# Kernel tuning notes

Hardware: AMD Instinct MI355X
Metric: run time of the kernel (lower is better)

Reference implementation:

```python
import jax, jax.numpy as jnp
import numpy as np

K = 7      # kernel_size
PAD = 3    # padding ('same' with stride 1)
G = 16     # groups


def _unfold(x):
    """torch nn.Unfold equivalent, stride=1, dilation=1.
    Returns [B, C, K*K, H, W] with kernel positions ordered (kh, kw),
    matching torch's (c, kh, kw) channel-major layout after reshape."""
    B, C, H, W = x.shape
    xp = jnp.pad(x, ((0, 0), (0, 0), (PAD, PAD), (PAD, PAD)))
    patches = jnp.stack(
        [xp[:, :, i:i + H, j:j + W] for i in range(K) for j in range(K)],
        axis=2,
    )
    return patches


def setup_inputs() -> dict:
    key = jax.random.key(0)
    k1, k2, k3 = jax.random.split(key, 3)
    B, C, H, W = 4, 256, 64, 64
    x = jax.random.normal(k1, (B, C, H, W), dtype=jnp.float32)
    # 1x1 conv producing kernel_prod*groups = 49*16 = 784 channels (with bias)
    w_kernel = jax.random.normal(k2, (G * K * K, C), dtype=jnp.float32) * 0.05
    b_kernel = jax.random.normal(k3, (G * K * K,), dtype=jnp.float32) * 0.05
    return {"x": x, "w_kernel": w_kernel, "b_kernel": b_kernel}


def reference(x, w_kernel, b_kernel):
    B, C, H, W = x.shape
    Cg = C // G
    # unfolded input: [B, G, C//G, K*K, H, W]
    patches = _unfold(x).reshape(B, G, Cg, K * K, H, W)
    # dynamic per-pixel kernel: AvgPool(k=1) is identity at stride 1,
    # then 1x1 conv with bias -> [B, G*K*K, H, W]
    kern = jnp.einsum('bchw,kc->bkhw', x, w_kernel) + b_kernel[None, :, None, None]
    kern = kern.reshape(B, G, 1, K * K, H, W)
    # multiply and sum-reduce over kernel positions, flatten groups
    out = (patches * kern).sum(axis=3).reshape(B, C, H, W)
    return out
```

## Files before the change

kernel.cpp:

```cpp
#include <hip/hip_runtime.h>


#define B_   4
#define C_   256
#define G_   16
#define KK_  49
#define KS_  7
#define PD_  3

#define XT_BYTES  (B_*4096*C_*2)
#define WBF_OFF   XT_BYTES

#define SKW   28
#define HC_   70
#define HPOS  (10*HC_)

typedef __attribute__((ext_vector_type(8))) short bf16x8;
typedef __attribute__((ext_vector_type(4))) float f32x4;
typedef unsigned short ushort_t;

__device__ inline unsigned f2bf(float f) {
    unsigned u = __float_as_uint(f);
    u += 0x7FFF + ((u >> 16) & 1);
    return u >> 16;
}

__global__ __launch_bounds__(256)
void cvt_xT(const float* __restrict__ x, const float* __restrict__ wk,
            ushort_t* __restrict__ xT, unsigned* __restrict__ wbf) {
    const int t = threadIdx.x;
    if (blockIdx.x == 64) {
        const int slice = blockIdx.z * 4 + blockIdx.y;
        const float2* wk2 = (const float2*)wk;
        const int base = slice * 6272;
        for (int k = t; k < 6272; k += 256) {
            float2 v = wk2[base + k];
            wbf[base + k] = f2bf(v.x) | (f2bf(v.y) << 16);
        }
        return;
    }
    __shared__ float tile[64][65];
    const int p0 = blockIdx.x * 64;
    const int c0 = blockIdx.y * 64;
    const int b  = blockIdx.z;
    const int px_r = t & 63;
    #pragma unroll
    for (int i = 0; i < 16; ++i) {
        int ch = (t >> 6) + i * 4;
        tile[ch][px_r] = x[((size_t)(b * C_ + c0 + ch) << 12) + p0 + px_r];
    }
    __syncthreads();
    const int px  = t >> 2;
    const int seg = t & 3;
    unsigned u[8];
    #pragma unroll
    for (int j = 0; j < 8; ++j) {
        float a0 = tile[seg * 16 + 2 * j][px];
        float a1 = tile[seg * 16 + 2 * j + 1][px];
        u[j] = f2bf(a0) | (f2bf(a1) << 16);
    }
    unsigned* dst = (unsigned*)(xT + ((size_t)((b << 12) + p0 + px)) * C_ + c0 + seg * 16);
    ((uint4*)dst)[0] = make_uint4(u[0], u[1], u[2], u[3]);
    ((uint4*)dst)[1] = make_uint4(u[4], u[5], u[6], u[7]);
}

__global__ __launch_bounds__(256, 4)
void inv_fused(const ushort_t* __restrict__ xT,
               const ushort_t* __restrict__ wbf,
               const float* __restrict__ bk,
               const float* __restrict__ x,
               float* __restrict__ out) {
    __shared__ unsigned kern2[256 * SKW];
    __shared__ unsigned halo4[HPOS * 4];

    const int bid  = blockIdx.x;
    const int g    = bid >> 6;
    const int b    = (bid >> 4) & 3;
    const int tile = bid & 15;
    const int gy0  = tile * 4;
    const int p0   = gy0 * 64;

    const int tid  = threadIdx.x;
    const int wv   = tid >> 6;
    const int ln15 = tid & 15;
    const int quad = (tid & 63) >> 4;

    f32x4 acc[16];
    #pragma unroll
    for (int i = 0; i < 16; ++i) acc[i] = (f32x4){0.f, 0.f, 0.f, 0.f};

    const ushort_t* ap[4];
    #pragma unroll
    for (int mt = 0; mt < 4; ++mt) {
        int r = mt * 16 + ln15; if (r > KK_ - 1) r = KK_ - 1;
        ap[mt] = wbf + (size_t)(g * KK_ + r) * C_ + quad * 8;
    }
    const ushort_t* bp = xT + ((size_t)((b << 12) + p0 + wv * 64 + ln15)) * C_ + quad * 8;

    bf16x8 af[2][4], bf[2][4];
    #pragma unroll
    for (int mt = 0; mt < 4; ++mt) af[0][mt] = *(const bf16x8*)(ap[mt]);
    #pragma unroll
    for (int nt = 0; nt < 4; ++nt) bf[0][nt] = *(const bf16x8*)(bp + nt * 16 * C_);

    #pragma unroll
    for (int k = 0; k < 8; ++k) {
        const int cur = k & 1, nxt = cur ^ 1;
        if (k < 7) {
            const int cc = (k + 1) * 32;
            #pragma unroll
            for (int mt = 0; mt < 4; ++mt)
                af[nxt][mt] = *(const bf16x8*)(ap[mt] + cc);
            #pragma unroll
            for (int nt = 0; nt < 4; ++nt)
                bf[nxt][nt] = *(const bf16x8*)(bp + nt * 16 * C_ + cc);
        }
        #pragma unroll
        for (int mt = 0; mt < 4; ++mt) {
            #pragma unroll
            for (int nt = 0; nt < 4; ++nt) {
                acc[mt * 4 + nt] = __builtin_amdgcn_mfma_f32_16x16x32_bf16(
                    af[cur][mt], bf[cur][nt], acc[mt * 4 + nt], 0, 0, 0);
            }
        }
    }

    #pragma unroll
    for (int mt = 0; mt < 3; ++mt) {
        const int m0 = mt * 16 + quad * 4;
        const float b0 = bk[g * KK_ + m0],     b1 = bk[g * KK_ + m0 + 1];
        const float b2 = bk[g * KK_ + m0 + 2], b3 = bk[g * KK_ + m0 + 3];
        #pragma unroll
        for (int nt = 0; nt < 4; ++nt) {
            const int p = wv * 64 + nt * 16 + ln15;
            uint2 d;
            d.x = f2bf(acc[mt * 4 + nt][0] + b0) | (f2bf(acc[mt * 4 + nt][1] + b1) << 16);
            d.y = f2bf(acc[mt * 4 + nt][2] + b2) | (f2bf(acc[mt * 4 + nt][3] + b3) << 16);
            *(uint2*)&kern2[p * SKW + mt * 8 + quad * 2] = d;
        }
    }
    if (quad == 0) {
        const float b48 = bk[g * KK_ + 48];
        #pragma unroll
        for (int nt = 0; nt < 4; ++nt) {
            const int p = wv * 64 + nt * 16 + ln15;
            kern2[p * SKW + 24] = f2bf(acc[12 + nt][0] + b48);
        }
    }
    __syncthreads();

    float kv[KK_];
    {
        const uint4* kr = (const uint4*)&kern2[tid * SKW];
        unsigned kd[28];
        #pragma unroll
        for (int q = 0; q < 7; ++q) {
            uint4 h = kr[q];
            kd[4*q] = h.x; kd[4*q+1] = h.y; kd[4*q+2] = h.z; kd[4*q+3] = h.w;
        }
        #pragma unroll
        for (int k = 0; k < KK_; ++k) {
            unsigned d = kd[k >> 1];
            kv[k] = __uint_as_float((k & 1) ? (d & 0xffff0000u) : (d << 16));
        }
    }

    const int py = tid >> 6, px = tid & 63;
    #pragma unroll 1
    for (int hb = 0; hb < 2; ++hb) {
        if (hb) __syncthreads();
        const int cbase = g * 16 + hb * 8;
        for (int e = tid; e < HPOS; e += 256) {
            int row = e / HC_;
            int col = e - row * HC_;
            int sy = gy0 + row - PD_;
            int sx = col - PD_;
            unsigned d0 = 0, d1 = 0, d2 = 0, d3 = 0;
            if (sy >= 0 && sy < 64 && sx >= 0 && sx < 64) {
                const float* xp = x + ((size_t)(b * C_ + cbase) << 12) + sy * 64 + sx;
                d0 = f2bf(xp[0])             | (f2bf(xp[1 << 12]) << 16);
                d1 = f2bf(xp[2 << 12])       | (f2bf(xp[3 << 12]) << 16);
                d2 = f2bf(xp[4 << 12])       | (f2bf(xp[5 << 12]) << 16);
                d3 = f2bf(xp[6 << 12])       | (f2bf(xp[7 << 12]) << 16);
            }
            *(uint4*)&halo4[e * 4] = make_uint4(d0, d1, d2, d3);
        }
        __syncthreads();

        float a[8];
        #pragma unroll
        for (int q = 0; q < 8; ++q) a[q] = 0.f;
        #pragma unroll
        for (int kh = 0; kh < KS_; ++kh) {
            const uint4* hr = (const uint4*)&halo4[(((py + kh) * HC_) + px) * 4];
            #pragma unroll
            for (int kw = 0; kw < KS_; ++kw) {
                uint4 hv = hr[kw];
                float kk = kv[kh * KS_ + kw];
                a[0] = fmaf(__uint_as_float(hv.x << 16),          kk, a[0]);
                a[1] = fmaf(__uint_as_float(hv.x & 0xffff0000u),  kk, a[1]);
                a[2] = fmaf(__uint_as_float(hv.y << 16),          kk, a[2]);
                a[3] = fmaf(__uint_as_float(hv.y & 0xffff0000u),  kk, a[3]);
                a[4] = fmaf(__uint_as_float(hv.z << 16),          kk, a[4]);
                a[5] = fmaf(__uint_as_float(hv.z & 0xffff0000u),  kk, a[5]);
                a[6] = fmaf(__uint_as_float(hv.w << 16),          kk, a[6]);
                a[7] = fmaf(__uint_as_float(hv.w & 0xffff0000u),  kk, a[7]);
            }
        }
        const size_t o = ((size_t)(b * C_ + cbase) << 12) + p0 + tid;
        #pragma unroll
        for (int q = 0; q < 8; ++q)
            out[o + ((size_t)q << 12)] = a[q];
    }
}

extern "C" void kernel_launch(void* const* d_in, const int* in_sizes, int n_in,
                              void* d_out, int out_size, void* d_ws, size_t ws_size,
                              hipStream_t stream) {
    const float* x  = (const float*)d_in[0];
    const float* wk = (const float*)d_in[1];
    const float* bk = (const float*)d_in[2];
    float* o = (float*)d_out;

    ushort_t* xT  = (ushort_t*)d_ws;
    unsigned* wbf = (unsigned*)((char*)d_ws + WBF_OFF);

    cvt_xT<<<dim3(65, 4, B_), dim3(256), 0, stream>>>(x, wk, xT, wbf);
    inv_fused<<<dim3(1024), dim3(256), 0, stream>>>(
        xT, (const ushort_t*)wbf, bk, x, o);
}
```

Before: 117.7 us.

## Halve pixel tile, load all 16 group channels in one halo pass

Each block now covers 2 output rows (128 pixels) instead of 4, so the grid doubles to 2048 blocks. The two threads per pixel split the 16 group channels into halves, and a single halo tile holds all 16 channels, which removes the second halo load and its extra barriers. The halo load now runs before the kernel-weight epilogue to overlap global loads with MFMA results, and launch bounds rise to 5 blocks per CU. In exchange, halo rows overlap more across tiles (8 rows per 2 output rows instead of 10 per 4), adding redundant x reads, and the weight matrix is re-read per smaller tile.

Result: slower. 128.4 us (+9.2%).

```diff
diff --git a/kernel.cpp b/kernel.cpp
--- a/kernel.cpp
+++ b/kernel.cpp
@@ -13,7 +13,8 @@
 
 #define SKW   28
 #define HC_   70
-#define HPOS  (10*HC_)
+#define HROWS 8
+#define HPOS  (HROWS*HC_)
 
 typedef __attribute__((ext_vector_type(8))) short bf16x8;
 typedef __attribute__((ext_vector_type(4))) float f32x4;
@@ -64,30 +65,31 @@
     ((uint4*)dst)[1] = make_uint4(u[4], u[5], u[6], u[7]);
 }
 
-__global__ __launch_bounds__(256, 4)
+__global__ __launch_bounds__(256, 5)
 void inv_fused(const ushort_t* __restrict__ xT,
                const ushort_t* __restrict__ wbf,
                const float* __restrict__ bk,
                const float* __restrict__ x,
                float* __restrict__ out) {
-    __shared__ unsigned kern2[256 * SKW];
-    __shared__ unsigned halo4[HPOS * 4];
+    __shared__ unsigned kern2[128 * SKW];
+    __shared__ unsigned halo8[HPOS * 8];
 
     const int bid  = blockIdx.x;
-    const int g    = bid >> 6;
-    const int b    = (bid >> 4) & 3;
-    const int tile = bid & 15;
-    const int gy0  = tile * 4;
-    const int p0   = gy0 * 64;
+    const int g    = bid >> 7;
+    const int rem  = bid & 127;
+    const int b    = rem >> 5;
+    const int tile = rem & 31;
+    const int gy0  = tile * 2;
+    const int p0   = tile * 128;
 
     const int tid  = threadIdx.x;
     const int wv   = tid >> 6;
     const int ln15 = tid & 15;
     const int quad = (tid & 63) >> 4;
 
-    f32x4 acc[16];
-    #pragma unroll
-    for (int i = 0; i < 16; ++i) acc[i] = (f32x4){0.f, 0.f, 0.f, 0.f};
+    f32x4 acc[8];
+    #pragma unroll
+    for (int i = 0; i < 8; ++i) acc[i] = (f32x4){0.f, 0.f, 0.f, 0.f};
 
     const ushort_t* ap[4];
     #pragma unroll
@@ -95,13 +97,13 @@
         int r = mt * 16 + ln15; if (r > KK_ - 1) r = KK_ - 1;
         ap[mt] = wbf + (size_t)(g * KK_ + r) * C_ + quad * 8;
     }
-    const ushort_t* bp = xT + ((size_t)((b << 12) + p0 + wv * 64 + ln15)) * C_ + quad * 8;
-
-    bf16x8 af[2][4], bf[2][4];
+    const ushort_t* bp = xT + ((size_t)((b << 12) + p0 + wv * 32 + ln15)) * C_ + quad * 8;
+
+    bf16x8 af[2][4], bf[2][2];
     #pragma unroll
     for (int mt = 0; mt < 4; ++mt) af[0][mt] = *(const bf16x8*)(ap[mt]);
     #pragma unroll
-    for (int nt = 0; nt < 4; ++nt) bf[0][nt] = *(const bf16x8*)(bp + nt * 16 * C_);
+    for (int nt = 0; nt < 2; ++nt) bf[0][nt] = *(const bf16x8*)(bp + nt * 16 * C_);
 
     #pragma unroll
     for (int k = 0; k < 8; ++k) {
@@ -112,17 +114,35 @@
             for (int mt = 0; mt < 4; ++mt)
                 af[nxt][mt] = *(const bf16x8*)(ap[mt] + cc);
             #pragma unroll
-            for (int nt = 0; nt < 4; ++nt)
+            for (int nt = 0; nt < 2; ++nt)
                 bf[nxt][nt] = *(const bf16x8*)(bp + nt * 16 * C_ + cc);
         }
         #pragma unroll
         for (int mt = 0; mt < 4; ++mt) {
             #pragma unroll
-            for (int nt = 0; nt < 4; ++nt) {
-                acc[mt * 4 + nt] = __builtin_amdgcn_mfma_f32_16x16x32_bf16(
-                    af[cur][mt], bf[cur][nt], acc[mt * 4 + nt], 0, 0, 0);
+            for (int nt = 0; nt < 2; ++nt) {
+                acc[mt * 2 + nt] = __builtin_amdgcn_mfma_f32_16x16x32_bf16(
+                    af[cur][mt], bf[cur][nt], acc[mt * 2 + nt], 0, 0, 0);
             }
         }
+    }
+
+    for (int e = tid; e < 2 * HPOS; e += 256) {
+        const int pos = e >> 1;
+        const int oct = e & 1;
+        const int row = pos / HC_;
+        const int col = pos - row * HC_;
+        const int sy = gy0 + row - PD_;
+        const int sx = col - PD_;
+        unsigned d0 = 0, d1 = 0, d2 = 0, d3 = 0;
+        if (sy >= 0 && sy < 64 && sx >= 0 && sx < 64) {
+            const float* xp = x + ((size_t)(b * C_ + g * 16 + oct * 8) << 12) + sy * 64 + sx;
+            d0 = f2bf(xp[0])       | (f2bf(xp[1 << 12]) << 16);
+            d1 = f2bf(xp[2 << 12]) | (f2bf(xp[3 << 12]) << 16);
+            d2 = f2bf(xp[4 << 12]) | (f2bf(xp[5 << 12]) << 16);
+            d3 = f2bf(xp[6 << 12]) | (f2bf(xp[7 << 12]) << 16);
+        }
+        *(uint4*)&halo8[pos * 8 + oct * 4] = make_uint4(d0, d1, d2, d3);
     }
 
     #pragma unroll
@@ -131,27 +151,29 @@
         const float b0 = bk[g * KK_ + m0],     b1 = bk[g * KK_ + m0 + 1];
         const float b2 = bk[g * KK_ + m0 + 2], b3 = bk[g * KK_ + m0 + 3];
         #pragma unroll
-        for (int nt = 0; nt < 4; ++nt) {
-            const int p = wv * 64 + nt * 16 + ln15;
+        for (int nt = 0; nt < 2; ++nt) {
+            const int p = wv * 32 + nt * 16 + ln15;
             uint2 d;
-            d.x = f2bf(acc[mt * 4 + nt][0] + b0) | (f2bf(acc[mt * 4 + nt][1] + b1) << 16);
-            d.y = f2bf(acc[mt * 4 + nt][2] + b2) | (f2bf(acc[mt * 4 + nt][3] + b3) << 16);
+            d.x = f2bf(acc[mt * 2 + nt][0] + b0) | (f2bf(acc[mt * 2 + nt][1] + b1) << 16);
+            d.y = f2bf(acc[mt * 2 + nt][2] + b2) | (f2bf(acc[mt * 2 + nt][3] + b3) << 16);
             *(uint2*)&kern2[p * SKW + mt * 8 + quad * 2] = d;
         }
     }
     if (quad == 0) {
         const float b48 = bk[g * KK_ + 48];
         #pragma unroll
-        for (int nt = 0; nt < 4; ++nt) {
-            const int p = wv * 64 + nt * 16 + ln15;
-            kern2[p * SKW + 24] = f2bf(acc[12 + nt][0] + b48);
+        for (int nt = 0; nt < 2; ++nt) {
+            const int p = wv * 32 + nt * 16 + ln15;
+            kern2[p * SKW + 24] = f2bf(acc[6 + nt][0] + b48);
         }
     }
     __syncthreads();
 
+    const int px7  = tid & 127;
+    const int half = tid >> 7;
     float kv[KK_];
     {
-        const uint4* kr = (const uint4*)&kern2[tid * SKW];
+        const uint4* kr = (const uint4*)&kern2[px7 * SKW];
         unsigned kd[28];
         #pragma unroll
         for (int q = 0; q < 7; ++q) {
@@ -165,53 +187,31 @@
         }
     }
 
-    const int py = tid >> 6, px = tid & 63;
-    #pragma unroll 1
-    for (int hb = 0; hb < 2; ++hb) {
-        if (hb) __syncthreads();
-        const int cbase = g * 16 + hb * 8;
-        for (int e = tid; e < HPOS; e += 256) {
-            int row = e / HC_;
-            int col = e - row * HC_;
-            int sy = gy0 + row - PD_;
-            int sx = col - PD_;
-            unsigned d0 = 0, d1 = 0, d2 = 0, d3 = 0;
-            if (sy >= 0 && sy < 64 && sx >= 0 && sx < 64) {
-                const float* xp = x + ((size_t)(b * C_ + cbase) << 12) + sy * 64 + sx;
-                d0 = f2bf(xp[0])             | (f2bf(xp[1 << 12]) << 16);
-                d1 = f2bf(xp[2 << 12])       | (f2bf(xp[3 << 12]) << 16);
-                d2 = f2bf(xp[4 << 12])       | (f2bf(xp[5 << 12]) << 16);
-                d3 = f2bf(xp[6 << 12])       | (f2bf(xp[7 << 12]) << 16);
-            }
-            *(uint4*)&halo4[e * 4] = make_uint4(d0, d1, d2, d3);
-        }
-        __syncthreads();
-
-        float a[8];
-        #pragma unroll
-        for (int q = 0; q < 8; ++q) a[q] = 0.f;
-        #pragma unroll
-        for (int kh = 0; kh < KS_; ++kh) {
-            const uint4* hr = (const uint4*)&halo4[(((py + kh) * HC_) + px) * 4];
-            #pragma unroll
-            for (int kw = 0; kw < KS_; ++kw) {
-                uint4 hv = hr[kw];
-                float kk = kv[kh * KS_ + kw];
-                a[0] = fmaf(__uint_as_float(hv.x << 16),          kk, a[0]);
-                a[1] = fmaf(__uint_as_float(hv.x & 0xffff0000u),  kk, a[1]);
-                a[2] = fmaf(__uint_as_float(hv.y << 16),          kk, a[2]);
-                a[3] = fmaf(__uint_as_float(hv.y & 0xffff0000u),  kk, a[3]);
-                a[4] = fmaf(__uint_as_float(hv.z << 16),          kk, a[4]);
-                a[5] = fmaf(__uint_as_float(hv.z & 0xffff0000u),  kk, a[5]);
-                a[6] = fmaf(__uint_as_float(hv.w << 16),          kk, a[6]);
-                a[7] = fmaf(__uint_as_float(hv.w & 0xffff0000u),  kk, a[7]);
-            }
-        }
-        const size_t o = ((size_t)(b * C_ + cbase) << 12) + p0 + tid;
-        #pragma unroll
-        for (int q = 0; q < 8; ++q)
-            out[o + ((size_t)q << 12)] = a[q];
-    }
+    const int row = px7 >> 6, col = px7 & 63;
+    float a[8];
+    #pragma unroll
+    for (int q = 0; q < 8; ++q) a[q] = 0.f;
+    #pragma unroll
+    for (int kh = 0; kh < KS_; ++kh) {
+        const uint4* hr = (const uint4*)&halo8[((row + kh) * HC_ + col) * 8 + half * 4];
+        #pragma unroll
+        for (int kw = 0; kw < KS_; ++kw) {
+            uint4 hv = hr[kw * 8 / 4];
+            float kk = kv[kh * KS_ + kw];
+            a[0] = fmaf(__uint_as_float(hv.x << 16),          kk, a[0]);
+            a[1] = fmaf(__uint_as_float(hv.x & 0xffff0000u),  kk, a[1]);
+            a[2] = fmaf(__uint_as_float(hv.y << 16),          kk, a[2]);
+            a[3] = fmaf(__uint_as_float(hv.y & 0xffff0000u),  kk, a[3]);
+            a[4] = fmaf(__uint_as_float(hv.z << 16),          kk, a[4]);
+            a[5] = fmaf(__uint_as_float(hv.z & 0xffff0000u),  kk, a[5]);
+            a[6] = fmaf(__uint_as_float(hv.w << 16),          kk, a[6]);
+            a[7] = fmaf(__uint_as_float(hv.w & 0xffff0000u),  kk, a[7]);
+        }
+    }
+    const size_t o = ((size_t)(b * C_ + g * 16 + half * 8) << 12) + p0 + px7;
+    #pragma unroll
+    for (int q = 0; q < 8; ++q)
+        out[o + ((size_t)q << 12)] = a[q];
 }
 
 extern "C" void kernel_launch(void* const* d_in, const int* in_sizes, int n_in,
@@ -226,6 +226,6 @@
     unsigned* wbf = (unsigned*)((char*)d_ws + WBF_OFF);
 
     cvt_xT<<<dim3(65, 4, B_), dim3(256), 0, stream>>>(x, wk, xT, wbf);
-    inv_fused<<<dim3(1024), dim3(256), 0, stream>>>(
+    inv_fused<<<dim3(2048), dim3(256), 0, stream>>>(
         xT, (const ushort_t*)wbf, bk, x, o);
 }
```

## Store bf16 input in channel-octet layout and prefetch halo from it

Applied to the files above, without the earlier changes.

The pre-conversion kernel now writes x as bf16 in an [B][C/8][pixel][8] layout instead of pixel-major with all channels. The fused kernel reads its GEMM B-operand and both halo tiles from that packed buffer with single 16-byte loads, rather than gathering eight strided fp32 values per halo position and converting them. The first halo is staged right after the MFMA loop, and the second half's halo is prefetched into registers before the first half's convolution runs. The cost is more register pressure, and the GEMM operand loads are now strided across octets rather than contiguous along channels.

Result: faster. 106.4 us (-9.6%).

```diff
diff --git a/kernel.cpp b/kernel.cpp
--- a/kernel.cpp
+++ b/kernel.cpp
@@ -8,8 +8,8 @@
 #define KS_  7
 #define PD_  3
 
-#define XT_BYTES  (B_*4096*C_*2)
-#define WBF_OFF   XT_BYTES
+#define XP8_BYTES (B_*32*4096*8*2)
+#define WBF_OFF   XP8_BYTES
 
 #define SKW   28
 #define HC_   70
@@ -26,8 +26,8 @@
 }
 
 __global__ __launch_bounds__(256)
-void cvt_xT(const float* __restrict__ x, const float* __restrict__ wk,
-            ushort_t* __restrict__ xT, unsigned* __restrict__ wbf) {
+void cvt_xp8(const float* __restrict__ x, const float* __restrict__ wk,
+             ushort_t* __restrict__ xp8, unsigned* __restrict__ wbf) {
     const int t = threadIdx.x;
     if (blockIdx.x == 64) {
         const int slice = blockIdx.z * 4 + blockIdx.y;
@@ -50,25 +50,38 @@
         tile[ch][px_r] = x[((size_t)(b * C_ + c0 + ch) << 12) + p0 + px_r];
     }
     __syncthreads();
-    const int px  = t >> 2;
-    const int seg = t & 3;
-    unsigned u[8];
-    #pragma unroll
-    for (int j = 0; j < 8; ++j) {
-        float a0 = tile[seg * 16 + 2 * j][px];
-        float a1 = tile[seg * 16 + 2 * j + 1][px];
-        u[j] = f2bf(a0) | (f2bf(a1) << 16);
-    }
-    unsigned* dst = (unsigned*)(xT + ((size_t)((b << 12) + p0 + px)) * C_ + c0 + seg * 16);
-    ((uint4*)dst)[0] = make_uint4(u[0], u[1], u[2], u[3]);
-    ((uint4*)dst)[1] = make_uint4(u[4], u[5], u[6], u[7]);
+    const int px = t & 63;
+    const int ob = t >> 6;
+    #pragma unroll
+    for (int jj = 0; jj < 2; ++jj) {
+        const int j = ob + jj * 4;
+        unsigned u[4];
+        #pragma unroll
+        for (int k2 = 0; k2 < 4; ++k2) {
+            float a0 = tile[j * 8 + 2 * k2][px];
+            float a1 = tile[j * 8 + 2 * k2 + 1][px];
+            u[k2] = f2bf(a0) | (f2bf(a1) << 16);
+        }
+        ushort_t* dst = xp8 + (((size_t)((b << 5) + (c0 >> 3) + j) << 12) + p0 + px) * 8;
+        *(uint4*)dst = make_uint4(u[0], u[1], u[2], u[3]);
+    }
+}
+
+__device__ inline uint4 stage_ld(const ushort_t* __restrict__ xp8,
+                                 int b, int oct, int gy0, int e) {
+    const int row = e / HC_;
+    const int col = e - row * HC_;
+    const int sy = gy0 + row - PD_;
+    const int sx = col - PD_;
+    if (sy >= 0 && sy < 64 && sx >= 0 && sx < 64)
+        return *(const uint4*)(xp8 + (((size_t)((b << 5) + oct) << 12) + sy * 64 + sx) * 8);
+    return make_uint4(0u, 0u, 0u, 0u);
 }
 
 __global__ __launch_bounds__(256, 4)
-void inv_fused(const ushort_t* __restrict__ xT,
+void inv_fused(const ushort_t* __restrict__ xp8,
                const ushort_t* __restrict__ wbf,
                const float* __restrict__ bk,
-               const float* __restrict__ x,
                float* __restrict__ out) {
     __shared__ unsigned kern2[256 * SKW];
     __shared__ unsigned halo4[HPOS * 4];
@@ -78,7 +91,7 @@
     const int b    = (bid >> 4) & 3;
     const int tile = bid & 15;
     const int gy0  = tile * 4;
-    const int p0   = gy0 * 64;
+    const int p0   = tile * 256;
 
     const int tid  = threadIdx.x;
     const int wv   = tid >> 6;
@@ -95,13 +108,13 @@
         int r = mt * 16 + ln15; if (r > KK_ - 1) r = KK_ - 1;
         ap[mt] = wbf + (size_t)(g * KK_ + r) * C_ + quad * 8;
     }
-    const ushort_t* bp = xT + ((size_t)((b << 12) + p0 + wv * 64 + ln15)) * C_ + quad * 8;
+    const ushort_t* bp = xp8 + (((size_t)((b << 5) + quad) << 12) + p0 + wv * 64 + ln15) * 8;
 
     bf16x8 af[2][4], bf[2][4];
     #pragma unroll
     for (int mt = 0; mt < 4; ++mt) af[0][mt] = *(const bf16x8*)(ap[mt]);
     #pragma unroll
-    for (int nt = 0; nt < 4; ++nt) bf[0][nt] = *(const bf16x8*)(bp + nt * 16 * C_);
+    for (int nt = 0; nt < 4; ++nt) bf[0][nt] = *(const bf16x8*)(bp + nt * 128);
 
     #pragma unroll
     for (int k = 0; k < 8; ++k) {
@@ -113,7 +126,7 @@
                 af[nxt][mt] = *(const bf16x8*)(ap[mt] + cc);
             #pragma unroll
             for (int nt = 0; nt < 4; ++nt)
-                bf[nxt][nt] = *(const bf16x8*)(bp + nt * 16 * C_ + cc);
+                bf[nxt][nt] = *(const bf16x8*)(bp + ((size_t)cc << 12) + nt * 128);
         }
         #pragma unroll
         for (int mt = 0; mt < 4; ++mt) {
@@ -124,6 +137,9 @@
             }
         }
     }
+
+    for (int e = tid; e < HPOS; e += 256)
+        *(uint4*)&halo4[e * 4] = stage_ld(xp8, b, 2 * g, gy0, e);
 
     #pragma unroll
     for (int mt = 0; mt < 3; ++mt) {
@@ -165,34 +181,28 @@
         }
     }
 
+    uint4 pf0 = stage_ld(xp8, b, 2 * g + 1, gy0, tid);
+    uint4 pf1 = stage_ld(xp8, b, 2 * g + 1, gy0, tid + 256);
+    uint4 pf2 = (tid < HPOS - 512) ? stage_ld(xp8, b, 2 * g + 1, gy0, tid + 512)
+                                   : make_uint4(0u, 0u, 0u, 0u);
+
     const int py = tid >> 6, px = tid & 63;
+
     #pragma unroll 1
     for (int hb = 0; hb < 2; ++hb) {
-        if (hb) __syncthreads();
-        const int cbase = g * 16 + hb * 8;
-        for (int e = tid; e < HPOS; e += 256) {
-            int row = e / HC_;
-            int col = e - row * HC_;
-            int sy = gy0 + row - PD_;
-            int sx = col - PD_;
-            unsigned d0 = 0, d1 = 0, d2 = 0, d3 = 0;
-            if (sy >= 0 && sy < 64 && sx >= 0 && sx < 64) {
-                const float* xp = x + ((size_t)(b * C_ + cbase) << 12) + sy * 64 + sx;
-                d0 = f2bf(xp[0])             | (f2bf(xp[1 << 12]) << 16);
-                d1 = f2bf(xp[2 << 12])       | (f2bf(xp[3 << 12]) << 16);
-                d2 = f2bf(xp[4 << 12])       | (f2bf(xp[5 << 12]) << 16);
-                d3 = f2bf(xp[6 << 12])       | (f2bf(xp[7 << 12]) << 16);
-            }
-            *(uint4*)&halo4[e * 4] = make_uint4(d0, d1, d2, d3);
-        }
-        __syncthreads();
-
+        if (hb) {
+            __syncthreads();
+            *(uint4*)&halo4[tid * 4] = pf0;
+            *(uint4*)&halo4[(tid + 256) * 4] = pf1;
+            if (tid < HPOS - 512) *(uint4*)&halo4[(tid + 512) * 4] = pf2;
+            __syncthreads();
+        }
         float a[8];
         #pragma unroll
         for (int q = 0; q < 8; ++q) a[q] = 0.f;
         #pragma unroll
         for (int kh = 0; kh < KS_; ++kh) {
-            const uint4* hr = (const uint4*)&halo4[(((py + kh) * HC_) + px) * 4];
+            const uint4* hr = (const uint4*)&halo4[((py + kh) * HC_ + px) * 4];
             #pragma unroll
             for (int kw = 0; kw < KS_; ++kw) {
                 uint4 hv = hr[kw];
@@ -207,7 +217,7 @@
                 a[7] = fmaf(__uint_as_float(hv.w & 0xffff0000u),  kk, a[7]);
             }
         }
-        const size_t o = ((size_t)(b * C_ + cbase) << 12) + p0 + tid;
+        const size_t o = ((size_t)(b * C_ + g * 16 + hb * 8) << 12) + p0 + tid;
         #pragma unroll
         for (int q = 0; q < 8; ++q)
             out[o + ((size_t)q << 12)] = a[q];
@@ -222,10 +232,10 @@
     const float* bk = (const float*)d_in[2];
     float* o = (float*)d_out;
 
-    ushort_t* xT  = (ushort_t*)d_ws;
+    ushort_t* xp8 = (ushort_t*)d_ws;
     unsigned* wbf = (unsigned*)((char*)d_ws + WBF_OFF);
 
-    cvt_xT<<<dim3(65, 4, B_), dim3(256), 0, stream>>>(x, wk, xT, wbf);
+    cvt_xp8<<<dim3(65, 4, B_), dim3(256), 0, stream>>>(x, wk, xp8, wbf);
     inv_fused<<<dim3(1024), dim3(256), 0, stream>>>(
-        xT, (const ushort_t*)wbf, bk, x, o);
-}
+        xp8, (const ushort_t*)wbf, bk, o);
+}
```
